# Kernel tuning notes

Hardware: AMD Instinct MI355X
Metric: run time of the kernel (lower is better)

The kernel has to match this reference:

```python
import jax, jax.numpy as jnp
import numpy as np

G = 7  # number of winner/loser assets

def setup_inputs() -> dict:
    key = jax.random.key(0)
    x = jax.random.normal(key, (4096, 8192, 1), dtype=jnp.float32)
    return {"x": x}

def reference(x):
    # x: [B, I, 1] -> [B, I]
    x = jnp.squeeze(x, axis=-1)
    # descending sort (argsort of -x gives descending order); gather values consistently
    sorted_indices = jnp.argsort(-x, axis=-1)                      # [B, I]
    sorted_x = jnp.take_along_axis(x, sorted_indices, axis=-1)     # [B, I] descending
    winner = jax.nn.softmax(sorted_x[:, :G], axis=-1)              # [B, G]
    loser = -jax.nn.softmax(1.0 - sorted_x[:, -G:], axis=-1)       # [B, G]
    zeros_mid = jnp.zeros_like(sorted_x[:, G:-G])                  # [B, I-2G]
    b_c = jnp.concatenate([winner, zeros_mid, loser], axis=1)      # [B, I]
    return (b_c, sorted_indices)
```

## Files before the change

kernel.cpp:

```cpp
#include <hip/hip_runtime.h>
#include <stdint.h>

#define N 8192
#define G 7
#define T 512
#define NW 8
typedef unsigned long long u64;
typedef uint32_t u32;

__device__ __forceinline__ u32 enc_desc(float x) {
    u32 u = __float_as_uint(x);
    return (u & 0x80000000u) ? u : (~u & 0x7FFFFFFFu);
}
__device__ __forceinline__ float dec_desc(u32 k) {
    u32 u = (k & 0x80000000u) ? k : (~k & 0x7FFFFFFFu);
    return __uint_as_float(u);
}

__global__ __launch_bounds__(T) void portfolio_radix_kernel(
    const float* __restrict__ x,
    float* __restrict__ bc,
    float* __restrict__ idx_out)
{
    __shared__ u64 data[N];
    __shared__ u32 wcnt[NW * 256];
    __shared__ u32 dsum[256];
    __shared__ u32 wsum[4];

    const int t    = threadIdx.x;
    const int w    = t >> 6;
    const int lane = t & 63;
    const int row  = blockIdx.x;
    const float* xr = x + (size_t)row * N;

    u64 key[16];
#pragma unroll
    for (int j = 0; j < 16; ++j) {
        int e = (w << 10) | (j << 6) | lane;
        key[j] = ((u64)enc_desc(xr[e]) << 32) | (u32)e;
    }

    u32 rank[16];

    for (int p = 0; p < 4; ++p) {
        const int shift = 8 * p;

#pragma unroll
        for (int i = 0; i < 4; ++i) wcnt[t + T * i] = 0;
        __syncthreads();

#pragma unroll
        for (int j = 0; j < 16; ++j) {
            u32 hi = (u32)(key[j] >> 32);
            u32 d  = (hi >> shift) & 255u;
            rank[j] = atomicAdd(&wcnt[(w << 8) | d], 1u);
        }
        __syncthreads();

        if (t < 256) {
            u32 run = 0;
#pragma unroll
            for (int ww = 0; ww < NW; ++ww) {
                u32 c = wcnt[(ww << 8) | t];
                wcnt[(ww << 8) | t] = run;
                run += c;
            }
            u32 v = run;
#pragma unroll
            for (int off = 1; off < 64; off <<= 1) {
                u32 u = __shfl_up(v, off, 64);
                if (lane >= off) v += u;
            }
            if (lane == 63) wsum[w] = v;
            dsum[t] = v - run;
        }
        __syncthreads();
        if (t < 256) {
            u32 add = 0;
            if (w > 0) add += wsum[0];
            if (w > 1) add += wsum[1];
            if (w > 2) add += wsum[2];
            dsum[t] += add;
        }
        __syncthreads();
#pragma unroll
        for (int i = 0; i < 4; ++i) {
            int id = t + T * i;
            wcnt[id] += dsum[id & 255];
        }
        __syncthreads();

#pragma unroll
        for (int j = 0; j < 16; ++j) {
            u32 hi = (u32)(key[j] >> 32);
            u32 d  = (hi >> shift) & 255u;
            rank[j] += wcnt[(w << 8) | d];
        }
#pragma unroll
        for (int j = 0; j < 16; ++j) data[rank[j]] = key[j];
        __syncthreads();

        if (p < 3) {
#pragma unroll
            for (int j = 0; j < 16; ++j) {
                int e = (w << 10) | (j << 6) | lane;
                key[j] = data[e];
            }
        }
    }

    float* bcr = bc + (size_t)row * N;
    float* ixr = idx_out + (size_t)row * N;
#pragma unroll
    for (int j = 0; j < 16; ++j) {
        int e = (w << 10) | (j << 6) | lane;
        u64 kk = data[e];
        ixr[e] = (float)(u32)(kk & 0xFFFFFFFFu);
        bcr[e] = 0.0f;
    }
    if (t < G) {
        float s[G], ex[G], sum = 0.f;
#pragma unroll
        for (int g = 0; g < G; ++g) s[g] = dec_desc((u32)(data[g] >> 32));
        float m0 = s[0];
#pragma unroll
        for (int g = 0; g < G; ++g) { ex[g] = expf(s[g] - m0); sum += ex[g]; }
        bcr[t] = ex[t] / sum;
    }
    if (t >= T - G) {
        float s[G], ex[G], sum = 0.f;
#pragma unroll
        for (int g = 0; g < G; ++g) s[g] = dec_desc((u32)(data[N - G + g] >> 32));
        float m0 = -s[G - 1];
#pragma unroll
        for (int g = 0; g < G; ++g) { ex[g] = expf(-s[g] - m0); sum += ex[g]; }
        bcr[(N - T) + t] = -ex[t - (T - G)] / sum;
    }
}

extern "C" void kernel_launch(void* const* d_in, const int* in_sizes, int n_in,
                              void* d_out, int out_size, void* d_ws, size_t ws_size,
                              hipStream_t stream) {
    const float* x = (const float*)d_in[0];
    float* out = (float*)d_out;
    const int B = in_sizes[0] / N;
    float* bc  = out;
    float* idx = out + (size_t)B * N;
    portfolio_radix_kernel<<<B, T, 0, stream>>>(x, bc, idx);
}
```

Before: 442.0 us.

## Shrink LDS footprint with split 32/16-bit keys and packed 16-bit radix counters

```diff
diff --git a/kernel.cpp b/kernel.cpp
--- a/kernel.cpp
+++ b/kernel.cpp
@@ -5,8 +5,8 @@
 #define G 7
 #define T 512
 #define NW 8
-typedef unsigned long long u64;
 typedef uint32_t u32;
+typedef uint16_t u16;
 
 __device__ __forceinline__ u32 enc_desc(float x) {
     u32 u = __float_as_uint(x);
@@ -17,43 +17,52 @@
     return __uint_as_float(u);
 }
 
-__global__ __launch_bounds__(T) void portfolio_radix_kernel(
+__global__ __launch_bounds__(T, 6) void portfolio_radix_kernel(
     const float* __restrict__ x,
     float* __restrict__ bc,
     float* __restrict__ idx_out)
 {
-    __shared__ u64 data[N];
-    __shared__ u32 wcnt[NW * 256];
-    __shared__ u32 dsum[256];
+    __shared__ u32 val_s[N];
+    __shared__ u16 idx_s[N];
+    __shared__ u16 wcnt[NW * 256];
+    __shared__ u16 dsum[256];
     __shared__ u32 wsum[4];
 
     const int t    = threadIdx.x;
     const int w    = t >> 6;
     const int lane = t & 63;
     const int row  = blockIdx.x;
-    const float* xr = x + (size_t)row * N;
+    const float* xr  = x + (size_t)row * N;
+    float* bcr = bc + (size_t)row * N;
+    float* ixr = idx_out + (size_t)row * N;
 
-    u64 key[16];
+    u32* wcnt32 = (u32*)wcnt;
+
+    u32 hi[16];
+    u32 lop[8];
+    u32 rnk[8];
 #pragma unroll
     for (int j = 0; j < 16; ++j) {
         int e = (w << 10) | (j << 6) | lane;
-        key[j] = ((u64)enc_desc(xr[e]) << 32) | (u32)e;
+        hi[j] = enc_desc(xr[e]);
+        if ((j & 1) == 0) lop[j >> 1] = (u32)e;
+        else              lop[j >> 1] |= ((u32)e) << 16;
+        if (e >= G && e < N - G) bcr[e] = 0.0f;
     }
-
-    u32 rank[16];
+    wcnt32[(w << 7) + lane] = 0;
+    wcnt32[(w << 7) + 64 + lane] = 0;
 
     for (int p = 0; p < 4; ++p) {
         const int shift = 8 * p;
 
 #pragma unroll
-        for (int i = 0; i < 4; ++i) wcnt[t + T * i] = 0;
-        __syncthreads();
-
-#pragma unroll
         for (int j = 0; j < 16; ++j) {
-            u32 hi = (u32)(key[j] >> 32);
-            u32 d  = (hi >> shift) & 255u;
-            rank[j] = atomicAdd(&wcnt[(w << 8) | d], 1u);
+            u32 d   = (hi[j] >> shift) & 255u;
+            u32 sh  = (d & 1u) << 4;
+            u32 ret = atomicAdd(&wcnt32[(w << 7) + (d >> 1)], 1u << sh);
+            u32 r   = (ret >> sh) & 0xFFFFu;
+            if ((j & 1) == 0) rnk[j >> 1] = r;
+            else              rnk[j >> 1] |= r << 16;
         }
         __syncthreads();
 
@@ -61,8 +70,8 @@
             u32 run = 0;
 #pragma unroll
             for (int ww = 0; ww < NW; ++ww) {
-                u32 c = wcnt[(ww << 8) | t];
-                wcnt[(ww << 8) | t] = run;
+                u32 c = (u32)wcnt[(ww << 8) | t];
+                wcnt[(ww << 8) | t] = (u16)run;
                 run += c;
             }
             u32 v = run;
@@ -72,56 +81,54 @@
                 if (lane >= off) v += u;
             }
             if (lane == 63) wsum[w] = v;
-            dsum[t] = v - run;
-        }
-        __syncthreads();
-        if (t < 256) {
-            u32 add = 0;
-            if (w > 0) add += wsum[0];
-            if (w > 1) add += wsum[1];
-            if (w > 2) add += wsum[2];
-            dsum[t] += add;
-        }
-        __syncthreads();
-#pragma unroll
-        for (int i = 0; i < 4; ++i) {
-            int id = t + T * i;
-            wcnt[id] += dsum[id & 255];
+            dsum[t] = (u16)(v - run);
         }
         __syncthreads();
 
+        {
+            u32 a0 = wsum[0], a1 = wsum[1], a2 = wsum[2];
+#pragma unroll
+            for (int i = 0; i < 4; ++i) {
+                int d = lane + (i << 6);
+                u32 addv = (i > 0 ? a0 : 0u) + (i > 1 ? a1 : 0u) + (i > 2 ? a2 : 0u);
+                wcnt[(w << 8) + d] = (u16)((u32)wcnt[(w << 8) + d] + (u32)dsum[d] + addv);
+            }
+        }
 #pragma unroll
         for (int j = 0; j < 16; ++j) {
-            u32 hi = (u32)(key[j] >> 32);
-            u32 d  = (hi >> shift) & 255u;
-            rank[j] += wcnt[(w << 8) | d];
+            u32 d   = (hi[j] >> shift) & 255u;
+            u32 sh  = ((u32)(j & 1)) << 4;
+            u32 pos = ((rnk[j >> 1] >> sh) & 0xFFFFu) + (u32)wcnt[(w << 8) + d];
+            u32 myi = (lop[j >> 1] >> sh) & 0xFFFFu;
+            if (p < 3 || pos < G || pos >= N - G) val_s[pos] = hi[j];
+            idx_s[pos] = (u16)myi;
         }
-#pragma unroll
-        for (int j = 0; j < 16; ++j) data[rank[j]] = key[j];
+        asm volatile("" ::: "memory");
+        wcnt32[(w << 7) + lane] = 0;
+        wcnt32[(w << 7) + 64 + lane] = 0;
         __syncthreads();
 
         if (p < 3) {
 #pragma unroll
             for (int j = 0; j < 16; ++j) {
                 int e = (w << 10) | (j << 6) | lane;
-                key[j] = data[e];
+                hi[j] = val_s[e];
+                u32 ii = (u32)idx_s[e];
+                if ((j & 1) == 0) lop[j >> 1] = ii;
+                else              lop[j >> 1] |= ii << 16;
             }
         }
     }
 
-    float* bcr = bc + (size_t)row * N;
-    float* ixr = idx_out + (size_t)row * N;
 #pragma unroll
     for (int j = 0; j < 16; ++j) {
         int e = (w << 10) | (j << 6) | lane;
-        u64 kk = data[e];
-        ixr[e] = (float)(u32)(kk & 0xFFFFFFFFu);
-        bcr[e] = 0.0f;
+        ixr[e] = (float)idx_s[e];
     }
     if (t < G) {
         float s[G], ex[G], sum = 0.f;
 #pragma unroll
-        for (int g = 0; g < G; ++g) s[g] = dec_desc((u32)(data[g] >> 32));
+        for (int g = 0; g < G; ++g) s[g] = dec_desc(val_s[g]);
         float m0 = s[0];
 #pragma unroll
         for (int g = 0; g < G; ++g) { ex[g] = expf(s[g] - m0); sum += ex[g]; }
@@ -130,7 +137,7 @@
     if (t >= T - G) {
         float s[G], ex[G], sum = 0.f;
 #pragma unroll
-        for (int g = 0; g < G; ++g) s[g] = dec_desc((u32)(data[N - G + g] >> 32));
+        for (int g = 0; g < G; ++g) s[g] = dec_desc(val_s[N - G + g]);
         float m0 = -s[G - 1];
 #pragma unroll
         for (int g = 0; g < G; ++g) { ex[g] = expf(-s[g] - m0); sum += ex[g]; }
```

New measurement: 519.8 us. 17.6% more time.
